# Kernel optimization log

Hardware: AMD Instinct MI355X
Metric: run time of the kernel (lower is better)

Reference implementation:

```python
import jax, jax.numpy as jnp
import numpy as np

D_MODEL = 512
N_HEADS = 8
HEAD_DIM = D_MODEL // N_HEADS


def setup_inputs() -> dict:
    key = jax.random.key(0)
    ks = jax.random.split(key, 9)
    B, S = 2, 2048
    s = 1.0 / np.sqrt(D_MODEL)
    return {
        "x": jax.random.normal(ks[0], (B, S, D_MODEL), dtype=jnp.float32),
        "wq": jax.random.uniform(ks[1], (D_MODEL, D_MODEL), jnp.float32, -s, s),
        "bq": jax.random.uniform(ks[2], (D_MODEL,), jnp.float32, -s, s),
        "wk": jax.random.uniform(ks[3], (D_MODEL, D_MODEL), jnp.float32, -s, s),
        "bk": jax.random.uniform(ks[4], (D_MODEL,), jnp.float32, -s, s),
        "wv": jax.random.uniform(ks[5], (D_MODEL, D_MODEL), jnp.float32, -s, s),
        "bv": jax.random.uniform(ks[6], (D_MODEL,), jnp.float32, -s, s),
        "wo": jax.random.uniform(ks[7], (D_MODEL, D_MODEL), jnp.float32, -s, s),
        "bo": jax.random.uniform(ks[8], (D_MODEL,), jnp.float32, -s, s),
    }


def reference(x, wq, bq, wk, bk, wv, bv, wo, bo):
    B, S, _ = x.shape
    # Linear layers (torch Linear: y = x @ W.T + b)
    q = x @ wq.T + bq
    k = x @ wk.T + bk
    v = x @ wv.T + bv
    # (B, H, S, Dh)
    def heads(t):
        return t.reshape(B, S, N_HEADS, HEAD_DIM).transpose(0, 2, 1, 3)
    q, k, v = heads(q), heads(k), heads(v)
    scale = 1.0 / np.sqrt(HEAD_DIM)
    scores = jnp.einsum("bhqd,bhkd->bhqk", q, k) * scale
    attn = jax.nn.softmax(scores, axis=-1)
    out = jnp.einsum("bhqk,bhkd->bhqd", attn, v)
    out = out.transpose(0, 2, 1, 3).reshape(B, S, D_MODEL)
    return out @ wo.T + bo
```

## Files before the change

### kernel.cpp

```cpp
#include <hip/hip_runtime.h>
#include <hip/hip_bf16.h>
#include <stdint.h>

typedef unsigned short u16;
typedef __attribute__((ext_vector_type(8))) short short8;
typedef __attribute__((ext_vector_type(4))) float f32x4;

#define AS1 __attribute__((address_space(1)))
#define AS3 __attribute__((address_space(3)))

__device__ __forceinline__ u16 f2bf(float f) {
    uint32_t u = __float_as_uint(f);
    u += 0x7fffu + ((u >> 16) & 1u);
    return (u16)(u >> 16);
}

__global__ __launch_bounds__(256) void cvt_kernel(
    const float* __restrict__ x, const float* __restrict__ wq,
    const float* __restrict__ wk, const float* __restrict__ wv,
    const float* __restrict__ wo, u16* __restrict__ dst)
{
    long e = ((long)blockIdx.x * 256 + threadIdx.x) * 8;
    const float* src; long off;
    if (e < 2097152L)      { src = x;  off = e; }
    else if (e < 2359296L) { src = wq; off = e - 2097152L; }
    else if (e < 2621440L) { src = wk; off = e - 2359296L; }
    else if (e < 2883584L) { src = wv; off = e - 2621440L; }
    else                   { src = wo; off = e - 2883584L; }
    float4 a = *(const float4*)(src + off);
    float4 b = *(const float4*)(src + off + 4);
    short8 v;
    v[0] = (short)f2bf(a.x); v[1] = (short)f2bf(a.y);
    v[2] = (short)f2bf(a.z); v[3] = (short)f2bf(a.w);
    v[4] = (short)f2bf(b.x); v[5] = (short)f2bf(b.y);
    v[6] = (short)f2bf(b.z); v[7] = (short)f2bf(b.w);
    *(short8*)(dst + e) = v;
}

__device__ __forceinline__ void gemm_core(
    const u16* __restrict__ A, const u16* __restrict__ Bm,
    int row0, int col0, u16* aSh, u16* bSh, int tid, f32x4 (&acc)[4][4])
{
    const int lane = tid & 63, w = tid >> 6;
    const int lg = lane >> 4, lj = lane & 15;
    const int wr = w >> 1, wc = w & 1;

    for (int ks = 0; ks < 8; ++ks) {
        const int k0 = ks * 64;
#pragma unroll
        for (int rd = 0; rd < 4; ++rd) {
            int t16 = rd * 256 + tid;
            int r = t16 >> 3, p = t16 & 7;
            int l = p ^ (r & 7);
            __builtin_amdgcn_global_load_lds(
                (const AS1 void*)(A + (size_t)(row0 + r) * 512 + k0 + l * 8),
                (AS3 void*)(aSh + t16 * 8), 16, 0, 0);
            __builtin_amdgcn_global_load_lds(
                (const AS1 void*)(Bm + (size_t)(col0 + r) * 512 + k0 + l * 8),
                (AS3 void*)(bSh + t16 * 8), 16, 0, 0);
        }
        __syncthreads();
#pragma unroll
        for (int kt = 0; kt < 2; ++kt) {
            short8 af[4], bf[4];
#pragma unroll
            for (int it = 0; it < 4; ++it) {
                int rowa = wr * 64 + it * 16 + lj;
                int c = kt * 4 + lg;
                af[it] = *(const short8*)((const char*)aSh + rowa * 128 + ((c ^ (rowa & 7)) << 4));
            }
#pragma unroll
            for (int jt = 0; jt < 4; ++jt) {
                int rowb = wc * 64 + jt * 16 + lj;
                int c = kt * 4 + lg;
                bf[jt] = *(const short8*)((const char*)bSh + rowb * 128 + ((c ^ (rowb & 7)) << 4));
            }
#pragma unroll
            for (int it = 0; it < 4; ++it)
#pragma unroll
                for (int jt = 0; jt < 4; ++jt)
                    acc[it][jt] = __builtin_amdgcn_mfma_f32_16x16x32_bf16(af[it], bf[jt], acc[it][jt], 0, 0, 0);
        }
        __syncthreads();
    }
}

__global__ __launch_bounds__(256) void gemm_qkv(
    const u16* __restrict__ xb, const u16* __restrict__ wqb, const u16* __restrict__ wvb,
    const float* __restrict__ bq, const float* __restrict__ bk, const float* __restrict__ bv,
    u16* __restrict__ Qb, u16* __restrict__ Kb, u16* __restrict__ Vtb)
{
    __shared__ u16 aSh[128 * 64];
    __shared__ u16 bSh[128 * 64];
    const int tid = threadIdx.x;
    const int lane = tid & 63, w = tid >> 6;
    const int lg = lane >> 4, lj = lane & 15;
    const int wr = w >> 1, wc = w & 1;
    const int id = blockIdx.x;

    f32x4 acc[4][4] = {};

    if (id < 256) {
        const int row0 = (id >> 3) * 128, col0 = (id & 7) * 128;
        gemm_core(xb, wqb, row0, col0, aSh, bSh, tid, acc);
#pragma unroll
        for (int jt = 0; jt < 4; ++jt) {
            int o = col0 + wc * 64 + jt * 16 + lj;
            float bias = (o < 512) ? bq[o] : bk[o - 512];
            float sc = (o < 512) ? 0.18033688011112042f : 1.0f;
            u16* base = (o < 512) ? Qb : Kb;
            int h = (o >> 6) & 7, d = o & 63;
#pragma unroll
            for (int it = 0; it < 4; ++it)
#pragma unroll
                for (int r = 0; r < 4; ++r) {
                    int n = row0 + wr * 64 + it * 16 + lg * 4 + r;
                    int b = n >> 11, s = n & 2047;
                    base[(size_t)(((b << 3) + h) * 2048 + s) * 64 + d] = f2bf((acc[it][jt][r] + bias) * sc);
                }
        }
    } else {
        const int idx = id - 256;
        const int row0 = (idx >> 5) * 128, col0 = (idx & 31) * 128;
        gemm_core(wvb, xb, row0, col0, aSh, bSh, tid, acc);
#pragma unroll
        for (int it = 0; it < 4; ++it)
#pragma unroll
            for (int r = 0; r < 4; ++r) {
                int orow = row0 + wr * 64 + it * 16 + lg * 4 + r;
                float bias = bv[orow];
#pragma unroll
                for (int jt = 0; jt < 4; ++jt) {
                    int n = col0 + wc * 64 + jt * 16 + lj;
                    Vtb[(size_t)orow * 4096 + n] = f2bf(acc[it][jt][r] + bias);
                }
            }
    }
}

__global__ __launch_bounds__(256) void gemm_out(
    const u16* __restrict__ A, const u16* __restrict__ Bm,
    const float* __restrict__ bias0, float* __restrict__ of32)
{
    __shared__ u16 aSh[128 * 64];
    __shared__ u16 bSh[128 * 64];
    const int tid = threadIdx.x;
    const int lane = tid & 63, w = tid >> 6;
    const int lg = lane >> 4, lj = lane & 15;
    const int wr = w >> 1, wc = w & 1;
    const int row0 = blockIdx.y * 128, col0 = blockIdx.x * 128;

    f32x4 acc[4][4] = {};
    gemm_core(A, Bm, row0, col0, aSh, bSh, tid, acc);

#pragma unroll
    for (int jt = 0; jt < 4; ++jt) {
        int o = col0 + wc * 64 + jt * 16 + lj;
        float bias = bias0[o];
#pragma unroll
        for (int it = 0; it < 4; ++it)
#pragma unroll
            for (int r = 0; r < 4; ++r) {
                int n = row0 + wr * 64 + it * 16 + lg * 4 + r;
                of32[(size_t)n * 512 + o] = acc[it][jt][r] + bias;
            }
    }
}

__global__ __launch_bounds__(256) void attn_kernel(
    const u16* __restrict__ Qb, const u16* __restrict__ Kb,
    const u16* __restrict__ Vtb, float* __restrict__ accP, float* __restrict__ lP)
{
    __shared__ u16 kvSh[2][2][32 * 64];
    __shared__ u16 pSh[4][16 * 40];
    const int tid = threadIdx.x;
    const int lane = tid & 63, w = tid >> 6;
    const int lg = lane >> 4, lj = lane & 15;
    const int bh = blockIdx.x, b = bh >> 3, h = bh & 7;
    const int z = blockIdx.z;
    const u16* Qh = Qb + (size_t)bh * 2048 * 64;
    const u16* Kh = Kb + (size_t)bh * 2048 * 64;
    const u16* Vh = Vtb + (size_t)h * 64 * 4096 + b * 2048;
    const int q0 = blockIdx.y * 64 + w * 16;
    const int kvbase = z * 512;
    u16* Pw = pSh[w];

#define STAGE(BUF, KV0) do {                                                              \
    {                                                                                     \
        int rk = tid >> 3, pk = tid & 7, lk = pk ^ (rk & 7);                              \
        __builtin_amdgcn_global_load_lds(                                                 \
            (const AS1 void*)(Kh + (size_t)((KV0) + rk) * 64 + lk * 8),                   \
            (AS3 void*)(kvSh[BUF][0] + tid * 8), 16, 0, 0);                               \
        int rv = tid >> 2, pv = tid & 3, lv = pv ^ ((rv >> 1) & 3);                       \
        __builtin_amdgcn_global_load_lds(                                                 \
            (const AS1 void*)(Vh + (size_t)rv * 4096 + (KV0) + lv * 8),                   \
            (AS3 void*)(kvSh[BUF][1] + tid * 8), 16, 0, 0);                               \
    }                                                                                     \
} while (0)

    short8 qf[2];
#pragma unroll
    for (int kt = 0; kt < 2; ++kt)
        qf[kt] = *(const short8*)(Qh + (size_t)(q0 + lj) * 64 + kt * 32 + lg * 8);

    const short8 vone = {0x3F80, 0x3F80, 0x3F80, 0x3F80, 0x3F80, 0x3F80, 0x3F80, 0x3F80};
    f32x4 accO[4] = {};
    f32x4 accO5 = {};

    STAGE(0, kvbase);
    __syncthreads();
    int buf = 0;
    for (int tt = 0; tt < 16; ++tt) {
        if (tt < 15) STAGE(buf ^ 1, kvbase + (tt + 1) * 32);
        const u16* Ksh = kvSh[buf][0];
        const u16* Vsh = kvSh[buf][1];
        f32x4 sf[2] = {};
#pragma unroll
        for (int kt = 0; kt < 2; ++kt) {
            int c = kt * 4 + lg;
#pragma unroll
            for (int jf = 0; jf < 2; ++jf) {
                int row = jf * 16 + lj;
                short8 kf = *(const short8*)((const char*)Ksh + row * 128 + ((c ^ (row & 7)) << 4));
                sf[jf] = __builtin_amdgcn_mfma_f32_16x16x32_bf16(qf[kt], kf, sf[jf], 0, 0, 0);
            }
        }
#pragma unroll
        for (int jf = 0; jf < 2; ++jf)
#pragma unroll
            for (int r = 0; r < 4; ++r) {
                float p = exp2f(sf[jf][r]);
                int row = lg * 4 + r;
                int phys = (jf * 2 + (lj >> 3)) ^ (row & 3);
                Pw[row * 40 + phys * 8 + (lj & 7)] = f2bf(p);
            }
        short8 pa = *(const short8*)((const char*)Pw + lj * 80 + ((lg ^ (lj & 3)) << 4));
        accO5 = __builtin_amdgcn_mfma_f32_16x16x32_bf16(pa, vone, accO5, 0, 0, 0);
#pragma unroll
        for (int jd = 0; jd < 4; ++jd) {
            int row = jd * 16 + lj;
            short8 vf = *(const short8*)((const char*)Vsh + row * 64 + ((lg ^ ((row >> 1) & 3)) << 4));
            accO[jd] = __builtin_amdgcn_mfma_f32_16x16x32_bf16(pa, vf, accO[jd], 0, 0, 0);
        }
        __syncthreads();
        buf ^= 1;
    }
#undef STAGE

    float* accW = accP + (size_t)z * 2097152;
#pragma unroll
    for (int r = 0; r < 4; ++r) {
        int q = q0 + lg * 4 + r;
        int s = b * 2048 + q;
#pragma unroll
        for (int jd = 0; jd < 4; ++jd)
            accW[(size_t)s * 512 + h * 64 + jd * 16 + lj] = accO[jd][r];
        if (lj == 0) lP[(z * 16 + bh) * 2048 + q] = accO5[r];
    }
}

__global__ __launch_bounds__(256) void combine_kernel(
    const float* __restrict__ accP, const float* __restrict__ lP, u16* __restrict__ Ob)
{
    int gid = blockIdx.x * 256 + threadIdx.x;
    int row = gid >> 6, cb = (gid & 63) * 8;
    int b = row >> 11, q = row & 2047;
    int h = (gid & 63) >> 3;
    int bh = b * 8 + h;
    float l = 0.0f;
#pragma unroll
    for (int z = 0; z < 4; ++z) l += lP[z * 32768 + bh * 2048 + q];
    float inv = 1.0f / l;
    float s[8] = {};
#pragma unroll
    for (int z = 0; z < 4; ++z) {
        const float* a = accP + (size_t)z * 2097152 + (size_t)row * 512 + cb;
        float4 x0 = *(const float4*)a, x1 = *(const float4*)(a + 4);
        s[0] += x0.x; s[1] += x0.y; s[2] += x0.z; s[3] += x0.w;
        s[4] += x1.x; s[5] += x1.y; s[6] += x1.z; s[7] += x1.w;
    }
    short8 o;
#pragma unroll
    for (int j = 0; j < 8; ++j) o[j] = (short)f2bf(s[j] * inv);
    *(short8*)(Ob + (size_t)gid * 8) = o;
}

extern "C" void kernel_launch(void* const* d_in, const int* in_sizes, int n_in,
                              void* d_out, int out_size, void* d_ws, size_t ws_size,
                              hipStream_t stream)
{
    const float* x  = (const float*)d_in[0];
    const float* wq = (const float*)d_in[1];
    const float* bq = (const float*)d_in[2];
    const float* wk = (const float*)d_in[3];
    const float* bk = (const float*)d_in[4];
    const float* wv = (const float*)d_in[5];
    const float* bv = (const float*)d_in[6];
    const float* wo = (const float*)d_in[7];
    const float* bo = (const float*)d_in[8];

    u16* w16 = (u16*)d_ws;
    u16* xb  = w16;
    u16* wqb = w16 + 2097152;
    u16* wvb = w16 + 2621440;
    u16* wob = w16 + 2883584;
    u16* Qb  = w16 + 3145728;
    u16* Kb  = w16 + 5242880;
    u16* Vtb = w16 + 7340032;
    u16* Ob  = w16 + 9437184;
    float* accPf = (float*)(w16 + 11534336);
    float* lPf   = accPf + 8388608;

    cvt_kernel<<<1536, 256, 0, stream>>>(x, wq, wk, wv, wo, w16);
    gemm_qkv<<<384, 256, 0, stream>>>(xb, wqb, wvb, bq, bk, bv, Qb, Kb, Vtb);
    attn_kernel<<<dim3(16, 32, 4), 256, 0, stream>>>(Qb, Kb, Vtb, accPf, lPf);
    combine_kernel<<<1024, 256, 0, stream>>>(accPf, lPf, Ob);
    gemm_out<<<dim3(4, 32), 256, 0, stream>>>(Ob, wob, bo, (float*)d_out);
}
```

Measured before the change: 83.93 us.

## Keep softmax probabilities in registers and double query rows per wave in attention

The attention kernel now computes S transposed (K as the A operand), so the exp'd probabilities come out in the register layout needed as the A operand of the PV MFMA. They are packed with v_cvt_pk_bf16_f32, which removes the LDS round trip for P. Each wave now handles 32 query rows, so every K/V fragment read from LDS feeds two MFMAs. The grid is halved to match, the loop is unrolled by two with fixed buffer offsets, and launch bounds request 4 blocks per CU. The costs are higher register pressure and fewer blocks in flight.

After: 72.72 us. -13.4%, faster.

```diff
diff --git a/kernel.cpp b/kernel.cpp
--- a/kernel.cpp
+++ b/kernel.cpp
@@ -5,6 +5,7 @@
 typedef unsigned short u16;
 typedef __attribute__((ext_vector_type(8))) short short8;
 typedef __attribute__((ext_vector_type(4))) float f32x4;
+typedef __attribute__((ext_vector_type(4))) unsigned int u32x4;
 
 #define AS1 __attribute__((address_space(1)))
 #define AS3 __attribute__((address_space(3)))
@@ -13,6 +14,12 @@
     uint32_t u = __float_as_uint(f);
     u += 0x7fffu + ((u >> 16) & 1u);
     return (u16)(u >> 16);
+}
+
+__device__ __forceinline__ uint32_t cvtpk(float a, float b) {
+    uint32_t r;
+    asm("v_cvt_pk_bf16_f32 %0, %1, %2" : "=v"(r) : "v"(a), "v"(b));
+    return r;
 }
 
 __global__ __launch_bounds__(256) void cvt_kernel(
@@ -167,12 +174,11 @@
     }
 }
 
-__global__ __launch_bounds__(256) void attn_kernel(
+__global__ __launch_bounds__(256, 4) void attn_kernel(
     const u16* __restrict__ Qb, const u16* __restrict__ Kb,
     const u16* __restrict__ Vtb, float* __restrict__ accP, float* __restrict__ lP)
 {
     __shared__ u16 kvSh[2][2][32 * 64];
-    __shared__ u16 pSh[4][16 * 40];
     const int tid = threadIdx.x;
     const int lane = tid & 63, w = tid >> 6;
     const int lg = lane >> 4, lj = lane & 15;
@@ -181,82 +187,108 @@
     const u16* Qh = Qb + (size_t)bh * 2048 * 64;
     const u16* Kh = Kb + (size_t)bh * 2048 * 64;
     const u16* Vh = Vtb + (size_t)h * 64 * 4096 + b * 2048;
-    const int q0 = blockIdx.y * 64 + w * 16;
+    const int q0 = blockIdx.y * 128 + w * 32;
     const int kvbase = z * 512;
-    u16* Pw = pSh[w];
-
-#define STAGE(BUF, KV0) do {                                                              \
-    {                                                                                     \
-        int rk = tid >> 3, pk = tid & 7, lk = pk ^ (rk & 7);                              \
-        __builtin_amdgcn_global_load_lds(                                                 \
-            (const AS1 void*)(Kh + (size_t)((KV0) + rk) * 64 + lk * 8),                   \
-            (AS3 void*)(kvSh[BUF][0] + tid * 8), 16, 0, 0);                               \
-        int rv = tid >> 2, pv = tid & 3, lv = pv ^ ((rv >> 1) & 3);                       \
-        __builtin_amdgcn_global_load_lds(                                                 \
-            (const AS1 void*)(Vh + (size_t)rv * 4096 + (KV0) + lv * 8),                   \
-            (AS3 void*)(kvSh[BUF][1] + tid * 8), 16, 0, 0);                               \
-    }                                                                                     \
-} while (0)
-
-    short8 qf[2];
+
+    int koff[2][2];
 #pragma unroll
     for (int kt = 0; kt < 2; ++kt)
-        qf[kt] = *(const short8*)(Qh + (size_t)(q0 + lj) * 64 + kt * 32 + lg * 8);
+#pragma unroll
+        for (int jf = 0; jf < 2; ++jf) {
+            int row = 8 * (lj >> 2) + 4 * jf + (lj & 3);
+            int sk = (row & 3) ^ (((row >> 3) & 3) << 1);
+            koff[kt][jf] = row * 128 + ((((kt * 4 + lg) ^ sk)) << 4);
+        }
+    int voff[4];
+#pragma unroll
+    for (int jd = 0; jd < 4; ++jd) {
+        int row = jd * 16 + lj;
+        voff[jd] = 4096 + row * 64 + ((lg ^ ((row >> 1) & 3)) << 4);
+    }
+
+    {
+    }
+    int r_ = tid >> 3, p_ = tid & 7;
+    int sk_ = (r_ & 3) ^ (((r_ >> 3) & 3) << 1);
+    const u16* Ks = Kh + (size_t)(kvbase + r_) * 64 + (p_ ^ sk_) * 8;
+    int rv_ = tid >> 2, pv_ = tid & 3;
+    const u16* Vs = Vh + (size_t)rv_ * 4096 + kvbase + (pv_ ^ ((rv_ >> 1) & 3)) * 8;
+    u16* kd0 = kvSh[0][0] + tid * 8;
+    u16* vd0 = kvSh[0][1] + tid * 8;
+
+#define STAGE(KD, VD) do {                                                    \
+    __builtin_amdgcn_global_load_lds((const AS1 void*)Ks, (AS3 void*)(KD), 16, 0, 0); \
+    __builtin_amdgcn_global_load_lds((const AS1 void*)Vs, (AS3 void*)(VD), 16, 0, 0); \
+    Ks += 2048; Vs += 32; } while (0)
+
+    short8 qf[2][2];
+#pragma unroll
+    for (int g = 0; g < 2; ++g)
+#pragma unroll
+        for (int kt = 0; kt < 2; ++kt)
+            qf[g][kt] = *(const short8*)(Qh + (size_t)(q0 + g * 16 + lj) * 64 + kt * 32 + lg * 8);
 
     const short8 vone = {0x3F80, 0x3F80, 0x3F80, 0x3F80, 0x3F80, 0x3F80, 0x3F80, 0x3F80};
-    f32x4 accO[4] = {};
-    f32x4 accO5 = {};
-
-    STAGE(0, kvbase);
+    f32x4 accO[2][4] = {};
+    f32x4 accO5[2] = {};
+
+    auto COMPUTE = [&](int ofs) {
+        const char* base = (const char*)kvSh + ofs;
+        f32x4 sf[2][2] = {};
+#pragma unroll
+        for (int kt = 0; kt < 2; ++kt) {
+            short8 kf0 = *(const short8*)(base + koff[kt][0]);
+            short8 kf1 = *(const short8*)(base + koff[kt][1]);
+            sf[0][0] = __builtin_amdgcn_mfma_f32_16x16x32_bf16(kf0, qf[0][kt], sf[0][0], 0, 0, 0);
+            sf[0][1] = __builtin_amdgcn_mfma_f32_16x16x32_bf16(kf1, qf[0][kt], sf[0][1], 0, 0, 0);
+            sf[1][0] = __builtin_amdgcn_mfma_f32_16x16x32_bf16(kf0, qf[1][kt], sf[1][0], 0, 0, 0);
+            sf[1][1] = __builtin_amdgcn_mfma_f32_16x16x32_bf16(kf1, qf[1][kt], sf[1][1], 0, 0, 0);
+        }
+        u32x4 t0, t1;
+        t0[0] = cvtpk(exp2f(sf[0][0][0]), exp2f(sf[0][0][1]));
+        t0[1] = cvtpk(exp2f(sf[0][0][2]), exp2f(sf[0][0][3]));
+        t0[2] = cvtpk(exp2f(sf[0][1][0]), exp2f(sf[0][1][1]));
+        t0[3] = cvtpk(exp2f(sf[0][1][2]), exp2f(sf[0][1][3]));
+        t1[0] = cvtpk(exp2f(sf[1][0][0]), exp2f(sf[1][0][1]));
+        t1[1] = cvtpk(exp2f(sf[1][0][2]), exp2f(sf[1][0][3]));
+        t1[2] = cvtpk(exp2f(sf[1][1][0]), exp2f(sf[1][1][1]));
+        t1[3] = cvtpk(exp2f(sf[1][1][2]), exp2f(sf[1][1][3]));
+        short8 pa0 = __builtin_bit_cast(short8, t0);
+        short8 pa1 = __builtin_bit_cast(short8, t1);
+        accO5[0] = __builtin_amdgcn_mfma_f32_16x16x32_bf16(pa0, vone, accO5[0], 0, 0, 0);
+        accO5[1] = __builtin_amdgcn_mfma_f32_16x16x32_bf16(pa1, vone, accO5[1], 0, 0, 0);
+#pragma unroll
+        for (int jd = 0; jd < 4; ++jd) {
+            short8 vf = *(const short8*)(base + voff[jd]);
+            accO[0][jd] = __builtin_amdgcn_mfma_f32_16x16x32_bf16(pa0, vf, accO[0][jd], 0, 0, 0);
+            accO[1][jd] = __builtin_amdgcn_mfma_f32_16x16x32_bf16(pa1, vf, accO[1][jd], 0, 0, 0);
+        }
+    };
+
+    STAGE(kd0, vd0);
     __syncthreads();
-    int buf = 0;
-    for (int tt = 0; tt < 16; ++tt) {
-        if (tt < 15) STAGE(buf ^ 1, kvbase + (tt + 1) * 32);
-        const u16* Ksh = kvSh[buf][0];
-        const u16* Vsh = kvSh[buf][1];
-        f32x4 sf[2] = {};
-#pragma unroll
-        for (int kt = 0; kt < 2; ++kt) {
-            int c = kt * 4 + lg;
-#pragma unroll
-            for (int jf = 0; jf < 2; ++jf) {
-                int row = jf * 16 + lj;
-                short8 kf = *(const short8*)((const char*)Ksh + row * 128 + ((c ^ (row & 7)) << 4));
-                sf[jf] = __builtin_amdgcn_mfma_f32_16x16x32_bf16(qf[kt], kf, sf[jf], 0, 0, 0);
-            }
-        }
-#pragma unroll
-        for (int jf = 0; jf < 2; ++jf)
-#pragma unroll
-            for (int r = 0; r < 4; ++r) {
-                float p = exp2f(sf[jf][r]);
-                int row = lg * 4 + r;
-                int phys = (jf * 2 + (lj >> 3)) ^ (row & 3);
-                Pw[row * 40 + phys * 8 + (lj & 7)] = f2bf(p);
-            }
-        short8 pa = *(const short8*)((const char*)Pw + lj * 80 + ((lg ^ (lj & 3)) << 4));
-        accO5 = __builtin_amdgcn_mfma_f32_16x16x32_bf16(pa, vone, accO5, 0, 0, 0);
-#pragma unroll
-        for (int jd = 0; jd < 4; ++jd) {
-            int row = jd * 16 + lj;
-            short8 vf = *(const short8*)((const char*)Vsh + row * 64 + ((lg ^ ((row >> 1) & 3)) << 4));
-            accO[jd] = __builtin_amdgcn_mfma_f32_16x16x32_bf16(pa, vf, accO[jd], 0, 0, 0);
-        }
+    for (int it = 0; it < 8; ++it) {
+        STAGE(kd0 + 4096, vd0 + 4096);
+        COMPUTE(0);
         __syncthreads();
-        buf ^= 1;
+        if (it < 7) STAGE(kd0, vd0);
+        COMPUTE(8192);
+        __syncthreads();
     }
 #undef STAGE
 
     float* accW = accP + (size_t)z * 2097152;
 #pragma unroll
-    for (int r = 0; r < 4; ++r) {
-        int q = q0 + lg * 4 + r;
-        int s = b * 2048 + q;
-#pragma unroll
-        for (int jd = 0; jd < 4; ++jd)
-            accW[(size_t)s * 512 + h * 64 + jd * 16 + lj] = accO[jd][r];
-        if (lj == 0) lP[(z * 16 + bh) * 2048 + q] = accO5[r];
-    }
+    for (int g = 0; g < 2; ++g)
+#pragma unroll
+        for (int r = 0; r < 4; ++r) {
+            int q = q0 + g * 16 + lg * 4 + r;
+            int s = b * 2048 + q;
+#pragma unroll
+            for (int jd = 0; jd < 4; ++jd)
+                accW[(size_t)s * 512 + h * 64 + jd * 16 + lj] = accO[g][jd][r];
+            if (lj == 0) lP[(z * 16 + bh) * 2048 + q] = accO5[g][r];
+        }
 }
 
 __global__ __launch_bounds__(256) void combine_kernel(
@@ -313,7 +345,7 @@
 
     cvt_kernel<<<1536, 256, 0, stream>>>(x, wq, wk, wv, wo, w16);
     gemm_qkv<<<384, 256, 0, stream>>>(xb, wqb, wvb, bq, bk, bv, Qb, Kb, Vtb);
-    attn_kernel<<<dim3(16, 32, 4), 256, 0, stream>>>(Qb, Kb, Vtb, accPf, lPf);
+    attn_kernel<<<dim3(16, 16, 4), 256, 0, stream>>>(Qb, Kb, Vtb, accPf, lPf);
     combine_kernel<<<1024, 256, 0, stream>>>(accPf, lPf, Ob);
     gemm_out<<<dim3(4, 32), 256, 0, stream>>>(Ob, wob, bo, (float*)d_out);
 }
```
